# Kernel tuning notes

Hardware: AMD Instinct MI355X
Metric: run time of the kernel (lower is better)

Reference implementation:

```python
import jax, jax.numpy as jnp
import numpy as np

N_VERT = 100000
N_EDGE = 1600000
D_E = 32
D_V = 64
D_G = 64
N_GRAPHS = 16
H = 256
D_OUT = 64


def setup_inputs() -> dict:
    key = jax.random.key(0)
    ks = jax.random.split(key, 12)
    v_attr = jax.random.normal(ks[0], (N_VERT, D_V), dtype=jnp.float32)
    edgeij_pair = jax.random.randint(ks[1], (2, N_EDGE), 0, N_VERT, dtype=jnp.int64)
    e_attr = jax.random.normal(ks[2], (N_EDGE, D_E), dtype=jnp.float32)
    g = jax.random.normal(ks[3], (N_GRAPHS, D_G), dtype=jnp.float32)
    batch = jnp.sort(jax.random.randint(ks[4], (N_VERT,), 0, N_GRAPHS, dtype=jnp.int64))
    n_in = D_V + 4 * D_E + D_G  # 256
    W1 = jax.random.normal(ks[5], (n_in, H), dtype=jnp.float32) * 0.05
    b1 = jnp.zeros((H,), dtype=jnp.float32)
    W2 = jax.random.normal(ks[6], (H, H), dtype=jnp.float32) * 0.05
    b2 = jnp.zeros((H,), dtype=jnp.float32)
    W3 = jax.random.normal(ks[7], (H, D_OUT), dtype=jnp.float32) * 0.05
    b3 = jnp.zeros((D_OUT,), dtype=jnp.float32)
    return {"v_attr": v_attr, "edgeij_pair": edgeij_pair, "e_attr": e_attr,
            "g": g, "batch": batch,
            "W1": W1, "b1": b1, "W2": W2, "b2": b2, "W3": W3, "b3": b3}


def reference(v_attr, edgeij_pair, e_attr, g, batch, W1, b1, W2, b2, W3, b3):
    n = v_attr.shape[0]
    src = edgeij_pair[0]
    # four segment reductions over the sending vertex (torch_scatter semantics:
    # empty segments produce 0 for min/max/mean/sum)
    agg_sum = jax.ops.segment_sum(e_attr, src, num_segments=n)
    cnt = jax.ops.segment_sum(jnp.ones((e_attr.shape[0], 1), e_attr.dtype), src, num_segments=n)
    agg_min = jax.ops.segment_min(e_attr, src, num_segments=n)
    agg_max = jax.ops.segment_max(e_attr, src, num_segments=n)
    has_edge = cnt > 0
    agg_min = jnp.where(has_edge, agg_min, 0.0)
    agg_max = jnp.where(has_edge, agg_max, 0.0)
    agg_mean = agg_sum / jnp.maximum(cnt, 1.0)
    agg = jnp.concatenate([agg_min, agg_mean, agg_sum, agg_max], axis=1)  # [N, 4*D_E]
    h = jnp.concatenate([v_attr, agg, g[batch]], axis=1)  # [N, D_V + 4*D_E + D_G]
    h = jax.nn.relu(h @ W1 + b1)
    h = jax.nn.relu(h @ W2 + b2)
    return h @ W3 + b3
```

## Files before the change

### kernel.cpp

```cpp
#include <hip/hip_runtime.h>

#define N_VERT 100000
#define N_EDGE 1600000

typedef __attribute__((ext_vector_type(8))) short short8;
typedef __attribute__((ext_vector_type(4))) float f32x4;

__device__ __forceinline__ unsigned short f2bf(float f) {
    unsigned int u = __float_as_uint(f);
    unsigned int r = (u + 0x7FFFu + ((u >> 16) & 1u)) >> 16;
    return (unsigned short)r;
}


__global__ void k_init(unsigned int* cnt) {
    int i = blockIdx.x * 256 + threadIdx.x;
    if (i < N_VERT) cnt[i] = 0u;
}

__global__ void k_count(const int* src, unsigned int* cnt) {
    int e = blockIdx.x * 256 + threadIdx.x;
    if (e < N_EDGE) atomicAdd(&cnt[src[e]], 1u);
}

__global__ void k_scan1(const unsigned int* cnt, unsigned int* off, unsigned int* part) {
    __shared__ unsigned int s[1024];
    int t = threadIdx.x;
    int i = blockIdx.x * 1024 + t;
    unsigned int v = (i < N_VERT) ? cnt[i] : 0u;
    s[t] = v;
    __syncthreads();
    for (int d = 1; d < 1024; d <<= 1) {
        unsigned int x = (t >= d) ? s[t - d] : 0u;
        __syncthreads();
        s[t] += x;
        __syncthreads();
    }
    if (i < N_VERT) off[i] = s[t] - v;
    if (t == 1023) part[blockIdx.x] = s[t];
}

__global__ void k_scan2(unsigned int* part) {
    __shared__ unsigned int s[128];
    int t = threadIdx.x;
    unsigned int v = (t < 98) ? part[t] : 0u;
    s[t] = v;
    __syncthreads();
    for (int d = 1; d < 128; d <<= 1) {
        unsigned int x = (t >= d) ? s[t - d] : 0u;
        __syncthreads();
        s[t] += x;
        __syncthreads();
    }
    part[t] = s[t] - v;
}

__global__ void k_addback(unsigned int* off, unsigned int* cur, const unsigned int* part) {
    int i = blockIdx.x * 256 + threadIdx.x;
    if (i < N_VERT) {
        unsigned int o = off[i] + part[i >> 10];
        off[i] = o;
        cur[i] = o;
    }
}

__global__ void k_place(const int* src, unsigned int* cur, unsigned int* eidx) {
    int e = blockIdx.x * 256 + threadIdx.x;
    if (e < N_EDGE) {
        unsigned int p = atomicAdd(&cur[src[e]], 1u);
        eidx[p] = (unsigned int)e;
    }
}

__global__ void k_wt(const float* W1, const float* W2, const float* W3,
                     unsigned short* W1t, unsigned short* W2t, unsigned short* W3t) {
    int t = blockIdx.x * 256 + threadIdx.x;
    if (t < 65536) {
        int n = t >> 8, k = t & 255;
        W1t[t] = f2bf(W1[k * 256 + n]);
    } else if (t < 131072) {
        int u = t - 65536;
        int n = u >> 8, k = u & 255;
        W2t[u] = f2bf(W2[k * 256 + n]);
    } else if (t < 147456) {
        int u = t - 131072;
        int n = u >> 8, k = u & 255;
        W3t[u] = f2bf(W3[k * 64 + n]);
    }
}


__device__ __forceinline__ void store8(unsigned char* base, int row, int feat0, const float* f) {
    union { short8 v; unsigned short u[8]; } p;
    for (int j = 0; j < 8; j++) p.u[j] = f2bf(f[j]);
    *(short8*)(base + row * 512 + ((feat0 * 2) ^ ((row & 7) << 4))) = p.v;
}

__device__ __forceinline__ void gemm_lds(const unsigned char* src, unsigned char* dst,
                                         const unsigned short* Wt, const float* bias,
                                         int NT, int tid) {
    int wave = tid >> 6, lane = tid & 63;
    int arow = wave * 16 + (lane & 15);
    int kb = (lane >> 4) * 8;
    int nl = lane & 15;
    int drow_base = wave * 16 + (lane >> 4) * 4;
    for (int nt = 0; nt < NT; ++nt) {
        float bv = bias[nt * 16 + nl];
        f32x4 acc = {bv, bv, bv, bv};
        const unsigned short* wp = Wt + (nt * 16 + nl) * 256 + kb;
        for (int k0 = 0; k0 < 8; k0++) {
            short8 a = *(const short8*)(src + arow * 512 + (((k0 * 32 + kb) * 2) ^ ((arow & 7) << 4)));
            short8 b = *(const short8*)(wp + k0 * 32);
            acc = __builtin_amdgcn_mfma_f32_16x16x32_bf16(a, b, acc, 0, 0, 0);
        }
        for (int i = 0; i < 4; i++) {
            float rv = acc[i];
            rv = rv > 0.f ? rv : 0.f;
            int row = drow_base + i;
            int col = nt * 16 + nl;
            *(unsigned short*)(dst + row * 512 + ((col * 2) ^ ((row & 7) << 4))) = f2bf(rv);
        }
    }
}

__global__ __launch_bounds__(256, 2) void k_mlp(
    const float* __restrict__ v_attr, const float* __restrict__ e_attr,
    const float* __restrict__ g, const int* __restrict__ batch,
    const unsigned int* __restrict__ cnt, const unsigned int* __restrict__ off,
    const unsigned int* __restrict__ eidx,
    const unsigned short* __restrict__ W1t, const unsigned short* __restrict__ W2t,
    const unsigned short* __restrict__ W3t,
    const float* __restrict__ b1, const float* __restrict__ b2, const float* __restrict__ b3,
    float* __restrict__ out)
{
    __shared__ __align__(16) unsigned char smem[65536];
    unsigned char* xs = smem;
    unsigned char* hs = smem + 32768;
    const int tid = threadIdx.x;
    const int v0 = blockIdx.x * 64;

    {
        int vl = tid >> 2, q = tid & 3;
        int v = v0 + vl;
        bool valid = v < N_VERT;
        float f[8];

        for (int c = 0; c < 2; c++) {
            int gi = q + c * 4;
            if (valid) {
                const float4* p = (const float4*)(v_attr + v * 64 + gi * 8);
                float4 a = p[0], b = p[1];
                f[0]=a.x; f[1]=a.y; f[2]=a.z; f[3]=a.w; f[4]=b.x; f[5]=b.y; f[6]=b.z; f[7]=b.w;
            } else {
                for (int j = 0; j < 8; j++) f[j] = 0.f;
            }
            store8(xs, vl, gi * 8, f);
        }

        float mn[8], mx[8], sm[8], me[8];
        for (int j = 0; j < 8; j++) { mn[j] = INFINITY; mx[j] = -INFINITY; sm[j] = 0.f; }
        unsigned int c_ = 0;
        if (valid) {
            c_ = cnt[v];
            unsigned int st = off[v];
            for (unsigned int j = 0; j < c_; j++) {
                unsigned int eid = eidx[st + j];
                const float4* p = (const float4*)(e_attr + eid * 32 + q * 8);
                float4 a = p[0], b = p[1];
                float t0[8] = {a.x, a.y, a.z, a.w, b.x, b.y, b.z, b.w};
                for (int jj = 0; jj < 8; jj++) {
                    float x = t0[jj];
                    mn[jj] = fminf(mn[jj], x);
                    mx[jj] = fmaxf(mx[jj], x);
                    sm[jj] += x;
                }
            }
        }
        if (c_ == 0) { for (int j = 0; j < 8; j++) { mn[j] = 0.f; mx[j] = 0.f; } }
        float inv = 1.0f / (float)(c_ > 1u ? c_ : 1u);
        for (int j = 0; j < 8; j++) me[j] = sm[j] * inv;
        store8(xs, vl,  64 + q * 8, mn);
        store8(xs, vl,  96 + q * 8, me);
        store8(xs, vl, 128 + q * 8, sm);
        store8(xs, vl, 160 + q * 8, mx);

        int b_ = valid ? batch[v] : 0;
        for (int c = 0; c < 2; c++) {
            int gi = q + c * 4;
            if (valid) {
                const float4* p = (const float4*)(g + b_ * 64 + gi * 8);
                float4 a = p[0], b = p[1];
                f[0]=a.x; f[1]=a.y; f[2]=a.z; f[3]=a.w; f[4]=b.x; f[5]=b.y; f[6]=b.z; f[7]=b.w;
            } else {
                for (int j = 0; j < 8; j++) f[j] = 0.f;
            }
            store8(xs, vl, 192 + gi * 8, f);
        }
    }
    __syncthreads();

    gemm_lds(xs, hs, W1t, b1, 16, tid);
    __syncthreads();
    gemm_lds(hs, xs, W2t, b2, 16, tid);
    __syncthreads();

    {
        int wave = tid >> 6, lane = tid & 63;
        int arow = wave * 16 + (lane & 15);
        int kb = (lane >> 4) * 8;
        int nl = lane & 15;
        for (int nt = 0; nt < 4; nt++) {
            float bv = b3[nt * 16 + nl];
            f32x4 acc = {bv, bv, bv, bv};
            const unsigned short* wp = W3t + (nt * 16 + nl) * 256 + kb;
            for (int k0 = 0; k0 < 8; k0++) {
                short8 a = *(const short8*)(xs + arow * 512 + (((k0 * 32 + kb) * 2) ^ ((arow & 7) << 4)));
                short8 b = *(const short8*)(wp + k0 * 32);
                acc = __builtin_amdgcn_mfma_f32_16x16x32_bf16(a, b, acc, 0, 0, 0);
            }
            for (int i = 0; i < 4; i++) {
                int row = wave * 16 + (lane >> 4) * 4 + i;
                int v = v0 + row;
                if (v < N_VERT) out[v * 64 + nt * 16 + nl] = acc[i];
            }
        }
    }
}


extern "C" void kernel_launch(void* const* d_in, const int* in_sizes, int n_in,
                              void* d_out, int out_size, void* d_ws, size_t ws_size,
                              hipStream_t stream) {
    const float* v_attr = (const float*)d_in[0];
    const int*   edge   = (const int*)d_in[1];
    const float* e_attr = (const float*)d_in[2];
    const float* g      = (const float*)d_in[3];
    const int*   batch  = (const int*)d_in[4];
    const float* W1 = (const float*)d_in[5];
    const float* b1 = (const float*)d_in[6];
    const float* W2 = (const float*)d_in[7];
    const float* b2 = (const float*)d_in[8];
    const float* W3 = (const float*)d_in[9];
    const float* b3 = (const float*)d_in[10];
    float* out = (float*)d_out;

    unsigned char* ws = (unsigned char*)d_ws;
    unsigned int*   cnt  = (unsigned int*)(ws + 0);
    unsigned int*   off  = (unsigned int*)(ws + 400000);
    unsigned int*   cur  = (unsigned int*)(ws + 800000);
    unsigned int*   eidx = (unsigned int*)(ws + 1200000);
    unsigned int*   part = (unsigned int*)(ws + 7600000);
    unsigned short* W1t  = (unsigned short*)(ws + 7600640);
    unsigned short* W2t  = (unsigned short*)(ws + 7731712);
    unsigned short* W3t  = (unsigned short*)(ws + 7862784);

    const int* src = edge;

    k_init   <<<391,  256,  0, stream>>>(cnt);
    k_count  <<<6250, 256,  0, stream>>>(src, cnt);
    k_scan1  <<<98,   1024, 0, stream>>>(cnt, off, part);
    k_scan2  <<<1,    128,  0, stream>>>(part);
    k_addback<<<391,  256,  0, stream>>>(off, cur, part);
    k_place  <<<6250, 256,  0, stream>>>(src, cur, eidx);
    k_wt     <<<576,  256,  0, stream>>>(W1, W2, W3, W1t, W2t, W3t);
    k_mlp    <<<1563, 256,  0, stream>>>(v_attr, e_attr, g, batch, cnt, off, eidx,
                                         W1t, W2t, W3t, b1, b2, b3, out);
}
```

Baseline: 798.6 us.

## Scatter edge attributes into CSR order as bf16 before aggregation

```diff
diff --git a/kernel.cpp b/kernel.cpp
--- a/kernel.cpp
+++ b/kernel.cpp
@@ -10,6 +10,9 @@
     unsigned int u = __float_as_uint(f);
     unsigned int r = (u + 0x7FFFu + ((u >> 16) & 1u)) >> 16;
     return (unsigned short)r;
+}
+__device__ __forceinline__ float bf2f(unsigned short u) {
+    return __uint_as_float(((unsigned int)u) << 16);
 }
 
 
@@ -61,6 +64,22 @@
         unsigned int o = off[i] + part[i >> 10];
         off[i] = o;
         cur[i] = o;
+    }
+}
+
+__global__ void k_reorder(const int* __restrict__ src, const float* __restrict__ e_attr,
+                          unsigned int* __restrict__ cur, unsigned short* __restrict__ es) {
+    int e = blockIdx.x * 256 + threadIdx.x;
+    if (e >= N_EDGE) return;
+    unsigned int p = atomicAdd(&cur[src[e]], 1u);
+    const float4* in = (const float4*)(e_attr + (size_t)e * 32);
+    unsigned short* op = es + (size_t)p * 32;
+    for (int h = 0; h < 4; h++) {
+        float4 a = in[h * 2], b = in[h * 2 + 1];
+        union { short8 v; unsigned short u[8]; } pk;
+        pk.u[0] = f2bf(a.x); pk.u[1] = f2bf(a.y); pk.u[2] = f2bf(a.z); pk.u[3] = f2bf(a.w);
+        pk.u[4] = f2bf(b.x); pk.u[5] = f2bf(b.y); pk.u[6] = f2bf(b.z); pk.u[7] = f2bf(b.w);
+        *(short8*)(op + h * 8) = pk.v;
     }
 }
 
@@ -123,8 +142,10 @@
     }
 }
 
+template <bool SORTED>
 __global__ __launch_bounds__(256, 2) void k_mlp(
     const float* __restrict__ v_attr, const float* __restrict__ e_attr,
+    const unsigned short* __restrict__ es,
     const float* __restrict__ g, const int* __restrict__ batch,
     const unsigned int* __restrict__ cnt, const unsigned int* __restrict__ off,
     const unsigned int* __restrict__ eidx,
@@ -148,7 +169,7 @@
         for (int c = 0; c < 2; c++) {
             int gi = q + c * 4;
             if (valid) {
-                const float4* p = (const float4*)(v_attr + v * 64 + gi * 8);
+                const float4* p = (const float4*)(v_attr + (size_t)v * 64 + gi * 8);
                 float4 a = p[0], b = p[1];
                 f[0]=a.x; f[1]=a.y; f[2]=a.z; f[3]=a.w; f[4]=b.x; f[5]=b.y; f[6]=b.z; f[7]=b.w;
             } else {
@@ -163,16 +184,30 @@
         if (valid) {
             c_ = cnt[v];
             unsigned int st = off[v];
-            for (unsigned int j = 0; j < c_; j++) {
-                unsigned int eid = eidx[st + j];
-                const float4* p = (const float4*)(e_attr + eid * 32 + q * 8);
-                float4 a = p[0], b = p[1];
-                float t0[8] = {a.x, a.y, a.z, a.w, b.x, b.y, b.z, b.w};
-                for (int jj = 0; jj < 8; jj++) {
-                    float x = t0[jj];
-                    mn[jj] = fminf(mn[jj], x);
-                    mx[jj] = fmaxf(mx[jj], x);
-                    sm[jj] += x;
+            if (SORTED) {
+                const unsigned short* ep = es + (size_t)st * 32 + q * 8;
+                for (unsigned int j = 0; j < c_; j++) {
+                    union { short8 v8; unsigned short u[8]; } r;
+                    r.v8 = *(const short8*)(ep + (size_t)j * 32);
+                    for (int jj = 0; jj < 8; jj++) {
+                        float x = bf2f(r.u[jj]);
+                        mn[jj] = fminf(mn[jj], x);
+                        mx[jj] = fmaxf(mx[jj], x);
+                        sm[jj] += x;
+                    }
+                }
+            } else {
+                for (unsigned int j = 0; j < c_; j++) {
+                    unsigned int eid = eidx[st + j];
+                    const float4* p = (const float4*)(e_attr + (size_t)eid * 32 + q * 8);
+                    float4 a = p[0], b = p[1];
+                    float t0[8] = {a.x, a.y, a.z, a.w, b.x, b.y, b.z, b.w};
+                    for (int jj = 0; jj < 8; jj++) {
+                        float x = t0[jj];
+                        mn[jj] = fminf(mn[jj], x);
+                        mx[jj] = fmaxf(mx[jj], x);
+                        sm[jj] += x;
+                    }
                 }
             }
         }
@@ -188,7 +223,7 @@
         for (int c = 0; c < 2; c++) {
             int gi = q + c * 4;
             if (valid) {
-                const float4* p = (const float4*)(g + b_ * 64 + gi * 8);
+                const float4* p = (const float4*)(g + (size_t)b_ * 64 + gi * 8);
                 float4 a = p[0], b = p[1];
                 f[0]=a.x; f[1]=a.y; f[2]=a.z; f[3]=a.w; f[4]=b.x; f[5]=b.y; f[6]=b.z; f[7]=b.w;
             } else {
@@ -221,7 +256,7 @@
             for (int i = 0; i < 4; i++) {
                 int row = wave * 16 + (lane >> 4) * 4 + i;
                 int v = v0 + row;
-                if (v < N_VERT) out[v * 64 + nt * 16 + nl] = acc[i];
+                if (v < N_VERT) out[(size_t)v * 64 + nt * 16 + nl] = acc[i];
             }
         }
     }
@@ -246,23 +281,36 @@
 
     unsigned char* ws = (unsigned char*)d_ws;
     unsigned int*   cnt  = (unsigned int*)(ws + 0);
-    unsigned int*   off  = (unsigned int*)(ws + 400000);
-    unsigned int*   cur  = (unsigned int*)(ws + 800000);
-    unsigned int*   eidx = (unsigned int*)(ws + 1200000);
-    unsigned int*   part = (unsigned int*)(ws + 7600000);
-    unsigned short* W1t  = (unsigned short*)(ws + 7600640);
-    unsigned short* W2t  = (unsigned short*)(ws + 7731712);
-    unsigned short* W3t  = (unsigned short*)(ws + 7862784);
+    unsigned int*   off  = (unsigned int*)(ws + 400384);
+    unsigned int*   cur  = (unsigned int*)(ws + 800768);
+    unsigned int*   part = (unsigned int*)(ws + 1201152);
+    unsigned short* W1t  = (unsigned short*)(ws + 1201664);
+    unsigned short* W2t  = (unsigned short*)(ws + 1332736);
+    unsigned short* W3t  = (unsigned short*)(ws + 1463808);
+    unsigned char*  tail = ws + 1496576;
+    const size_t NEED_SORTED = 1496576ull + (size_t)N_EDGE * 64ull;
 
     const int* src = edge;
+    const bool sorted = ws_size >= NEED_SORTED;
 
     k_init   <<<391,  256,  0, stream>>>(cnt);
     k_count  <<<6250, 256,  0, stream>>>(src, cnt);
     k_scan1  <<<98,   1024, 0, stream>>>(cnt, off, part);
     k_scan2  <<<1,    128,  0, stream>>>(part);
     k_addback<<<391,  256,  0, stream>>>(off, cur, part);
-    k_place  <<<6250, 256,  0, stream>>>(src, cur, eidx);
     k_wt     <<<576,  256,  0, stream>>>(W1, W2, W3, W1t, W2t, W3t);
-    k_mlp    <<<1563, 256,  0, stream>>>(v_attr, e_attr, g, batch, cnt, off, eidx,
-                                         W1t, W2t, W3t, b1, b2, b3, out);
-}
+
+    if (sorted) {
+        unsigned short* es = (unsigned short*)tail;
+        k_reorder<<<6250, 256, 0, stream>>>(src, e_attr, cur, es);
+        k_mlp<true><<<1563, 256, 0, stream>>>(v_attr, e_attr, es, g, batch, cnt, off,
+                                              (const unsigned int*)nullptr,
+                                              W1t, W2t, W3t, b1, b2, b3, out);
+    } else {
+        unsigned int* eidx = (unsigned int*)tail;
+        k_place<<<6250, 256, 0, stream>>>(src, cur, eidx);
+        k_mlp<false><<<1563, 256, 0, stream>>>(v_attr, e_attr, (const unsigned short*)nullptr,
+                                               g, batch, cnt, off, eidx,
+                                               W1t, W2t, W3t, b1, b2, b3, out);
+    }
+}
```

New measurement: 712.8 us. -10.7%, faster.
